# Kernel optimization log

Hardware: AMD Instinct MI355X
Metric: run time of the kernel (lower is better)

## Reference

```python
import jax, jax.numpy as jnp
import numpy as np

KSIZE = 5
PAD = 2  # replicate padding per side for 'same' 5x5x5 box filter


def setup_inputs() -> dict:
    key = jax.random.key(0)
    # mp: [N, C, D, H, W] nonnegative probability maps
    mp = jax.random.uniform(key, (1, 21, 16, 256, 256), dtype=jnp.float32)
    return {"mp": mp}


def reference(mp):
    N, C, D, H, W = mp.shape
    # replicate ('edge') padding on D, H, W, then depthwise 5x5x5 box filter
    x = jnp.pad(mp, ((0, 0), (0, 0), (PAD, PAD), (PAD, PAD), (PAD, PAD)), mode="edge")
    k = jnp.full((C, 1, KSIZE, KSIZE, KSIZE), 1.0 / (KSIZE ** 3), dtype=mp.dtype)
    y = jax.lax.conv_general_dilated(
        x, k,
        window_strides=(1, 1, 1),
        padding="VALID",
        dimension_numbers=("NCDHW", "OIDHW", "NCDHW"),
        feature_group_count=C,
    )  # [N, C, D, H, W]

    # normalize over channel axis (torch permutes to put channels first; we keep axis=1)
    y = y / jnp.sum(y, axis=1, keepdims=True)

    # weighted-median selection: running cumulative sum over channels
    s = jnp.cumsum(y, axis=1)                     # [N, C, D, H, W]
    idx = jnp.arange(C).reshape(1, C, 1, 1, 1)    # channel indices

    # med0: LAST channel i with y[i] > 0 and cumsum < 0.5 (torch loop overwrites), default 0
    med0 = jnp.maximum(
        jnp.max(jnp.where((y > 0) & (s < 0.5), idx, -1), axis=1, keepdims=True), 0
    )
    # med1: torch sets med[1] only while med[1]==0, so the result is the FIRST
    # NONZERO channel with cumsum > 0.5 (i=0 qualifying leaves med[1]==0 and gets
    # overwritten by the next qualifying i); 0 if no nonzero channel qualifies.
    med1 = jnp.argmax((s > 0.5) & (idx > 0), axis=1, keepdims=True)

    keep = (idx == med0) | (idx == med1)
    return jnp.where(keep, y, jnp.zeros((), dtype=y.dtype))
```

## Files before the change

kernel.cpp:

```cpp
#include <hip/hip_runtime.h>

#define CC   21
#define DD   16
#define HH   256
#define WW   256
#define HWP  (HH * WW)
#define DHW  (DD * HWP)

typedef float f4a __attribute__((ext_vector_type(4), aligned(16)));
__device__ __forceinline__ f4a f4add(f4a a, f4a b) { return a + b; }

#define AROW 36
#define PYN  12
#define A_SZ (DD * PYN * AROW)

#define NT1  (8 * 32 * CC)
#define G1   1280

__global__ __launch_bounds__(256, 5) void dh_blur_kernel(const float* __restrict__ mp,
                                                         float* __restrict__ out) {
    __shared__ float A[A_SZ];
    const int tid = threadIdx.x;

    const int s   = (tid >= 96) ? 1 : 0;
    const int col = (tid < 192) ? (tid - s * 96) : 0;
    const int py  = col >> 3;
    const int x4  = col & 7;

    for (int t = blockIdx.x; t < NT1; t += G1) {
        const int xb = t & 7;
        const int yb = (t >> 3) & 31;
        const int ch = t >> 8;
        const int w0 = xb * 32;
        const int h0 = yb * 8;
        const float* __restrict__ src = mp + (size_t)ch * DHW;

        if (tid < 192) {
            const int h = min(HH - 1, max(0, h0 + py - 2));
            const float* colp = src + (size_t)h * WW + w0 + x4 * 4;

            f4a l[12];
#pragma unroll
            for (int m = 0; m < 12; ++m) {
                const int dz = s * 8 + m;
                const int d  = min(DD - 1, max(0, dz - 2));
                l[m] = *(const f4a*)(colp + (size_t)d * HWP);
            }
            f4a sum = f4add(f4add(f4add(l[0], l[1]), f4add(l[2], l[3])), l[4]);
#pragma unroll
            for (int i = 0; i < 8; ++i) {
                *(f4a*)(&A[((s * 8 + i) * PYN + py) * AROW + x4 * 4]) = sum;
                if (i < 7) sum = sum - l[i] + l[i + 5];
            }
        }
        __syncthreads();

#pragma unroll
        for (int it = 0; it < 4; ++it) {
            const int tt   = tid + it * 256;
            const int xx4  = tt & 7;
            const int y    = (tt >> 3) & 7;
            const int dout = tt >> 6;

            const float* b = &A[(dout * PYN + y) * AROW + xx4 * 4];
            f4a a = *(const f4a*)b;
#pragma unroll
            for (int k = 1; k < 5; ++k) a = f4add(a, *(const f4a*)(b + k * AROW));

            *(f4a*)(out + (size_t)ch * DHW + (size_t)dout * HWP
                    + (h0 + y) * WW + w0 + xx4 * 4) = a;
        }
        __syncthreads();
    }
}

#define ROWP 264

#define NT2  (HH * DD)
#define G2   1792

__global__ __launch_bounds__(256, 7) void wmedian_kernel(float* __restrict__ y4) {
    __shared__ float R[CC * ROWP];
    const int tid = threadIdx.x;

    for (int t = blockIdx.x; t < NT2; t += G2) {
        const int h = t & 255;
        const int d = t >> 8;
        float* __restrict__ base = y4 + (size_t)d * HWP + (size_t)h * WW;

        for (int idx = tid; idx < CC * 64; idx += 256) {
            const int c  = idx >> 6;
            const int w4 = idx & 63;
            *(f4a*)(&R[c * ROWP + 4 + w4 * 4]) =
                *(const f4a*)(base + (size_t)c * DHW + w4 * 4);
        }
        if (tid < CC) {
            const float v0 = base[(size_t)tid * DHW];
            const float vL = base[(size_t)tid * DHW + (WW - 1)];
            R[tid * ROWP + 2]   = v0;
            R[tid * ROWP + 3]   = v0;
            R[tid * ROWP + 260] = vL;
            R[tid * ROWP + 261] = vL;
        }
        __syncthreads();

        const int w = tid;
        float v[CC];
        float tot = 0.f;
#pragma unroll
        for (int c = 0; c < CC; ++c) {
            const float* r = &R[c * ROWP + 2 + w];
            v[c] = ((((r[0] + r[1]) + r[2]) + r[3]) + r[4]);
            tot += v[c];
        }
        const float inv = 1.0f / tot;

        float ss = 0.f, sv0 = 0.f, sv1 = 0.f;
        int m0 = 0, m1 = 0;
#pragma unroll
        for (int c = 0; c < CC; ++c) {
            const float yn = v[c] * inv;
            const float sn = ss + yn;
            if (c == 0) { sv0 = yn; sv1 = yn; }
            if (v[c] > 0.f && sn < 0.5f) { m0 = c; sv0 = yn; }
            if (m1 == 0 && c > 0 && sn > 0.5f) { m1 = c; sv1 = yn; }
            ss = sn;
        }

#pragma unroll
        for (int c = 0; c < CC; ++c) {
            base[(size_t)c * DHW + w] = (c == m0) ? sv0 : ((c == m1) ? sv1 : 0.f);
        }
        __syncthreads();
    }
}

extern "C" void kernel_launch(void* const* d_in, const int* in_sizes, int n_in,
                              void* d_out, int out_size, void* d_ws, size_t ws_size,
                              hipStream_t stream) {
    const float* mp = (const float*)d_in[0];
    float* out = (float*)d_out;

    dh_blur_kernel<<<G1, 256, 0, stream>>>(mp, out);
    wmedian_kernel<<<G2, 256, 0, stream>>>(out);
}
```

Baseline: 196.3 us.

## Prefetch next blur tile into registers and rewrite median pass without shared memory

The blur kernel now issues the global loads for the next tile before the barrier, so they overlap with the shared-memory reduction and stores of the current tile. Its barriers become a raw s_barrier after waiting only on LDS counters, so outstanding global loads are not drained. The weighted-median kernel drops its shared-memory row staging and persistent loop: each thread handles 4 consecutive W pixels, doing float4 loads plus float2 halo loads with edge replication in registers, and writes float4 results. This costs more registers (12 float4 prefetch buffers, 84 floats per median thread) and lower occupancy bounds in return for fewer barriers and wider memory accesses.

```diff
diff --git a/kernel.cpp b/kernel.cpp
--- a/kernel.cpp
+++ b/kernel.cpp
@@ -8,7 +8,15 @@
 #define DHW  (DD * HWP)
 
 typedef float f4a __attribute__((ext_vector_type(4), aligned(16)));
+typedef float f2a __attribute__((ext_vector_type(2), aligned(8)));
 __device__ __forceinline__ f4a f4add(f4a a, f4a b) { return a + b; }
+
+#define BAR()                                                \
+    do {                                                     \
+        asm volatile("s_waitcnt lgkmcnt(0)" ::: "memory");   \
+        __builtin_amdgcn_s_barrier();                        \
+        asm volatile("" ::: "memory");                       \
+    } while (0)
 
 #define AROW 36
 #define PYN  12
@@ -17,15 +25,34 @@
 #define NT1  (8 * 32 * CC)
 #define G1   1280
 
+__device__ __forceinline__ void issue_tile_loads(const float* __restrict__ mp,
+                                                 int t, int s, int py, int x4,
+                                                 f4a (&L)[12]) {
+    const int xb = t & 7;
+    const int yb = (t >> 3) & 31;
+    const int ch = t >> 8;
+    const int h  = min(HH - 1, max(0, yb * 8 + py - 2));
+    const float* colp = mp + (size_t)ch * DHW + (size_t)h * WW + xb * 32 + x4 * 4;
+#pragma unroll
+    for (int m = 0; m < 12; ++m) {
+        const int dz = s * 8 + m;
+        const int d  = min(DD - 1, max(0, dz - 2));
+        L[m] = *(const f4a*)(colp + (size_t)d * HWP);
+    }
+}
+
 __global__ __launch_bounds__(256, 5) void dh_blur_kernel(const float* __restrict__ mp,
                                                          float* __restrict__ out) {
     __shared__ float A[A_SZ];
     const int tid = threadIdx.x;
-
     const int s   = (tid >= 96) ? 1 : 0;
     const int col = (tid < 192) ? (tid - s * 96) : 0;
     const int py  = col >> 3;
     const int x4  = col & 7;
+    const bool ldr = (tid < 192);
+
+    f4a L[12];
+    if (ldr) issue_tile_loads(mp, blockIdx.x, s, py, x4, L);
 
     for (int t = blockIdx.x; t < NT1; t += G1) {
         const int xb = t & 7;
@@ -33,27 +60,20 @@
         const int ch = t >> 8;
         const int w0 = xb * 32;
         const int h0 = yb * 8;
-        const float* __restrict__ src = mp + (size_t)ch * DHW;
 
-        if (tid < 192) {
-            const int h = min(HH - 1, max(0, h0 + py - 2));
-            const float* colp = src + (size_t)h * WW + w0 + x4 * 4;
-
-            f4a l[12];
-#pragma unroll
-            for (int m = 0; m < 12; ++m) {
-                const int dz = s * 8 + m;
-                const int d  = min(DD - 1, max(0, dz - 2));
-                l[m] = *(const f4a*)(colp + (size_t)d * HWP);
-            }
-            f4a sum = f4add(f4add(f4add(l[0], l[1]), f4add(l[2], l[3])), l[4]);
+        if (ldr) {
+            f4a sum = f4add(f4add(f4add(L[0], L[1]), f4add(L[2], L[3])), L[4]);
 #pragma unroll
             for (int i = 0; i < 8; ++i) {
                 *(f4a*)(&A[((s * 8 + i) * PYN + py) * AROW + x4 * 4]) = sum;
-                if (i < 7) sum = sum - l[i] + l[i + 5];
+                if (i < 7) sum = sum - L[i] + L[i + 5];
             }
         }
-        __syncthreads();
+
+        const int tn = t + G1;
+        if (tn < NT1 && ldr) issue_tile_loads(mp, tn, s, py, x4, L);
+
+        BAR();
 
 #pragma unroll
         for (int it = 0; it < 4; ++it) {
@@ -70,68 +90,64 @@
             *(f4a*)(out + (size_t)ch * DHW + (size_t)dout * HWP
                     + (h0 + y) * WW + w0 + xx4 * 4) = a;
         }
-        __syncthreads();
+
+        BAR();
     }
 }
 
-#define ROWP 264
+__global__ __launch_bounds__(256, 4) void wmedian_kernel(float* __restrict__ y4) {
+    const int g = blockIdx.x * 256 + threadIdx.x;
+    const int q = g & 63;
+    const size_t base = (size_t)g * 4;
 
-#define NT2  (HH * DD)
-#define G2   1792
+    float v[CC][4];
+    float tot[4] = {0.f, 0.f, 0.f, 0.f};
+#pragma unroll
+    for (int c = 0; c < CC; ++c) {
+        const float* p = y4 + (size_t)c * DHW + base;
+        const f4a M = *(const f4a*)(p);
+        f2a l2 = *(const f2a*)(p + ((q == 0) ? 0 : -2));
+        f2a r2 = *(const f2a*)(p + ((q == 63) ? 0 : 4));
+        if (q == 0)  { l2.x = M.x; l2.y = M.x; }
+        if (q == 63) { r2.x = M.w; r2.y = M.w; }
+        const float e0 = l2.x, e1 = l2.y, e2 = M.x, e3 = M.y;
+        const float e4 = M.z,  e5 = M.w,  e6 = r2.x, e7 = r2.y;
+        v[c][0] = ((((e0 + e1) + e2) + e3) + e4);
+        v[c][1] = ((((e1 + e2) + e3) + e4) + e5);
+        v[c][2] = ((((e2 + e3) + e4) + e5) + e6);
+        v[c][3] = ((((e3 + e4) + e5) + e6) + e7);
+#pragma unroll
+        for (int pp = 0; pp < 4; ++pp) tot[pp] += v[c][pp];
+    }
 
-__global__ __launch_bounds__(256, 7) void wmedian_kernel(float* __restrict__ y4) {
-    __shared__ float R[CC * ROWP];
-    const int tid = threadIdx.x;
+    float inv[4];
+#pragma unroll
+    for (int pp = 0; pp < 4; ++pp) inv[pp] = 1.0f / tot[pp];
 
-    for (int t = blockIdx.x; t < NT2; t += G2) {
-        const int h = t & 255;
-        const int d = t >> 8;
-        float* __restrict__ base = y4 + (size_t)d * HWP + (size_t)h * WW;
-
-        for (int idx = tid; idx < CC * 64; idx += 256) {
-            const int c  = idx >> 6;
-            const int w4 = idx & 63;
-            *(f4a*)(&R[c * ROWP + 4 + w4 * 4]) =
-                *(const f4a*)(base + (size_t)c * DHW + w4 * 4);
+    float sacc[4] = {0.f, 0.f, 0.f, 0.f};
+    float v0[4], v1[4];
+    int m0[4] = {0, 0, 0, 0}, m1[4] = {0, 0, 0, 0};
+#pragma unroll
+    for (int c = 0; c < CC; ++c) {
+#pragma unroll
+        for (int pp = 0; pp < 4; ++pp) {
+            const float yn = v[c][pp] * inv[pp];
+            const float sn = sacc[pp] + yn;
+            if (c == 0) { v0[pp] = yn; v1[pp] = yn; }
+            if (v[c][pp] > 0.f && sn < 0.5f) { m0[pp] = c; v0[pp] = yn; }
+            if (m1[pp] == 0 && c > 0 && sn > 0.5f) { m1[pp] = c; v1[pp] = yn; }
+            sacc[pp] = sn;
         }
-        if (tid < CC) {
-            const float v0 = base[(size_t)tid * DHW];
-            const float vL = base[(size_t)tid * DHW + (WW - 1)];
-            R[tid * ROWP + 2]   = v0;
-            R[tid * ROWP + 3]   = v0;
-            R[tid * ROWP + 260] = vL;
-            R[tid * ROWP + 261] = vL;
-        }
-        __syncthreads();
-
-        const int w = tid;
-        float v[CC];
-        float tot = 0.f;
-#pragma unroll
-        for (int c = 0; c < CC; ++c) {
-            const float* r = &R[c * ROWP + 2 + w];
-            v[c] = ((((r[0] + r[1]) + r[2]) + r[3]) + r[4]);
-            tot += v[c];
-        }
-        const float inv = 1.0f / tot;
-
-        float ss = 0.f, sv0 = 0.f, sv1 = 0.f;
-        int m0 = 0, m1 = 0;
-#pragma unroll
-        for (int c = 0; c < CC; ++c) {
-            const float yn = v[c] * inv;
-            const float sn = ss + yn;
-            if (c == 0) { sv0 = yn; sv1 = yn; }
-            if (v[c] > 0.f && sn < 0.5f) { m0 = c; sv0 = yn; }
-            if (m1 == 0 && c > 0 && sn > 0.5f) { m1 = c; sv1 = yn; }
-            ss = sn;
-        }
+    }
 
 #pragma unroll
-        for (int c = 0; c < CC; ++c) {
-            base[(size_t)c * DHW + w] = (c == m0) ? sv0 : ((c == m1) ? sv1 : 0.f);
-        }
-        __syncthreads();
+    for (int c = 0; c < CC; ++c) {
+        f4a o;
+        o.x = (c == m0[0]) ? v0[0] : ((c == m1[0]) ? v1[0] : 0.f);
+        o.y = (c == m0[1]) ? v0[1] : ((c == m1[1]) ? v1[1] : 0.f);
+        o.z = (c == m0[2]) ? v0[2] : ((c == m1[2]) ? v1[2] : 0.f);
+        o.w = (c == m0[3]) ? v0[3] : ((c == m1[3]) ? v1[3] : 0.f);
+        *(f4a*)(y4 + (size_t)c * DHW + base) = o;
     }
 }
 
@@ -142,5 +158,5 @@
     float* out = (float*)d_out;
 
     dh_blur_kernel<<<G1, 256, 0, stream>>>(mp, out);
-    wmedian_kernel<<<G2, 256, 0, stream>>>(out);
+    wmedian_kernel<<<(DHW / 4) / 256, 256, 0, stream>>>(out);
 }
```

Result: no change. 197.8 us (+0.8%).
